# Kernel tuning notes

Measured on AMD Instinct MI355X. Metric: run time of the kernel, lower is better.

The kernel has to match this reference:

```python
import jax, jax.numpy as jnp
import numpy as np
from jax import lax

B, T, N = 256, 2048, 64  # batch, max_seq_len, num_tags


def setup_inputs() -> dict:
    key = jax.random.key(0)
    k1, k2, k3 = jax.random.split(key, 3)
    x = jax.random.normal(k1, (B, T, N), dtype=jnp.float32)
    seq_len = jax.random.randint(k2, (B,), 1, T + 1).astype(jnp.int32)
    trans = (jax.random.normal(k3, (N, N), dtype=jnp.float32) * 0.1)
    return {"x": x, "seq_len": seq_len, "trans": trans}


def reference(x, seq_len, trans):
    # Viterbi decode (tfa.text.crf_decode): returns (tags [B,T] int32, scores [B] float)
    Bv, Tv, Nv = x.shape
    alpha0 = x[:, 0]                                   # [B,N]
    xs = jnp.swapaxes(x[:, 1:], 0, 1)                  # [T-1,B,N]
    valid = jnp.arange(1, Tv)[:, None] < seq_len[None, :]  # [T-1,B]
    ident = jnp.arange(Nv, dtype=jnp.int32)

    def fwd(alpha, inp):
        x_t, v = inp
        # scores[b, prev, cur] = alpha[b, prev] + trans[prev, cur]
        sc = alpha[:, :, None] + trans[None]           # [B,N,N]
        bp = jnp.argmax(sc, axis=1).astype(jnp.int32)  # [B,N] best prev tag per cur
        new_alpha = jnp.max(sc, axis=1) + x_t          # [B,N]
        # steps beyond seq_len: carry state, identity backpointer
        alpha_n = jnp.where(v[:, None], new_alpha, alpha)
        bp = jnp.where(v[:, None], bp, ident[None, :])
        return alpha_n, bp

    alpha_f, bps = lax.scan(fwd, alpha0, (xs, valid))  # bps: [T-1,B,N]
    scores = jnp.max(alpha_f, axis=-1)                 # [B]
    last = jnp.argmax(alpha_f, axis=-1).astype(jnp.int32)  # [B] tag at last step

    def bwd(tag, bp):
        prev = jnp.take_along_axis(bp, tag[:, None], axis=1)[:, 0]
        return prev, tag  # emit tag at step t+1, carry tag at step t

    first, rest = lax.scan(bwd, last, bps, reverse=True)   # rest: [T-1,B]
    tags = jnp.concatenate([first[:, None], jnp.swapaxes(rest, 0, 1)], axis=1)  # [B,T]
    return tags, scores
```

## Files before the change

kernel.cpp:

```cpp
#include <hip/hip_runtime.h>

#define BB 256
#define TT 2048
#define NN 64
#define CHK 512

template <int K>
__device__ __forceinline__ int dpp_ror_i(int v) {
  return __builtin_amdgcn_update_dpp(0, v, 0x120 | K, 0xF, 0xF, true);
}
template <int K>
__device__ __forceinline__ float dpp_ror_f(float v) {
  return __int_as_float(dpp_ror_i<K>(__float_as_int(v)));
}

__device__ __forceinline__ float rowpair_max(float m) {
  int a = __float_as_int(m), b = a;
  asm volatile("v_permlane16_swap_b32 %0, %1" : "+v"(a), "+v"(b));
  float fa = __int_as_float(a), fb = __int_as_float(b);
  return fmaxf(fa, fb);
}
__device__ __forceinline__ float half_max(float m) {
  int a = __float_as_int(m), b = a;
  asm volatile("v_permlane32_swap_b32 %0, %1" : "+v"(a), "+v"(b));
  float fa = __int_as_float(a), fb = __int_as_float(b);
  return fmaxf(fa, fb);
}
__device__ __forceinline__ int rowpair_min(int v) {
  int a = v, b = v;
  asm volatile("v_permlane16_swap_b32 %0, %1" : "+v"(a), "+v"(b));
  return a < b ? a : b;
}
__device__ __forceinline__ int half_min(int v) {
  int a = v, b = v;
  asm volatile("v_permlane32_swap_b32 %0, %1" : "+v"(a), "+v"(b));
  return a < b ? a : b;
}

__global__ __launch_bounds__(256, 1)
void crf_viterbi_kernel(const float* __restrict__ x,
                        const int* __restrict__ seq_len,
                        const float* __restrict__ trans,
                        float* __restrict__ out) {
  const int b = blockIdx.x;
  const int tid = threadIdx.x;
  const int lane = tid & 63;
  const int w = tid >> 6;
  const int c = lane & 15;
  const int jc = (w << 4) + c;

  __shared__ __align__(16) float alpha_s[2][NN];
  __shared__ unsigned char bp_s[(TT - 1) * NN];
  __shared__ int map_s[4][NN];

  const float* xb = x + (size_t)b * TT * NN;
  const int slen = seq_len[b];

  int idxv[16];
  idxv[0] = lane;
  idxv[1] = dpp_ror_i<1>(lane);   idxv[2] = dpp_ror_i<2>(lane);
  idxv[3] = dpp_ror_i<3>(lane);   idxv[4] = dpp_ror_i<4>(lane);
  idxv[5] = dpp_ror_i<5>(lane);   idxv[6] = dpp_ror_i<6>(lane);
  idxv[7] = dpp_ror_i<7>(lane);   idxv[8] = dpp_ror_i<8>(lane);
  idxv[9] = dpp_ror_i<9>(lane);   idxv[10] = dpp_ror_i<10>(lane);
  idxv[11] = dpp_ror_i<11>(lane); idxv[12] = dpp_ror_i<12>(lane);
  idxv[13] = dpp_ror_i<13>(lane); idxv[14] = dpp_ror_i<14>(lane);
  idxv[15] = dpp_ror_i<15>(lane);

  float tcv[16];
#pragma unroll
  for (int k = 0; k < 16; ++k) tcv[k] = trans[idxv[k] * NN + jc];

  if (w == 0) alpha_s[0][lane] = xb[lane];
  __syncthreads();

  float xn1 = xb[NN + jc];
  float xn2 = xb[2 * NN + jc];

  for (int t = 1; t < slen; ++t) {
    float xv = xn1;
    xn1 = xn2;
    {
      int tn = (t + 2 < TT) ? (t + 2) : (TT - 1);
      xn2 = xb[(size_t)tn * NN + jc];
    }
    const int pr = (t + 1) & 1;
    const int pw = t & 1;

    float av = alpha_s[pr][lane];

    float c0 = av + tcv[0];
    float c1 = dpp_ror_f<1>(av) + tcv[1];
    float c2 = dpp_ror_f<2>(av) + tcv[2];
    float c3 = dpp_ror_f<3>(av) + tcv[3];
    float c4 = dpp_ror_f<4>(av) + tcv[4];
    float c5 = dpp_ror_f<5>(av) + tcv[5];
    float c6 = dpp_ror_f<6>(av) + tcv[6];
    float c7 = dpp_ror_f<7>(av) + tcv[7];
    float c8 = dpp_ror_f<8>(av) + tcv[8];
    float c9 = dpp_ror_f<9>(av) + tcv[9];
    float c10 = dpp_ror_f<10>(av) + tcv[10];
    float c11 = dpp_ror_f<11>(av) + tcv[11];
    float c12 = dpp_ror_f<12>(av) + tcv[12];
    float c13 = dpp_ror_f<13>(av) + tcv[13];
    float c14 = dpp_ror_f<14>(av) + tcv[14];
    float c15 = dpp_ror_f<15>(av) + tcv[15];

    float m = fmaxf(fmaxf(fmaxf(fmaxf(c0, c1), fmaxf(c2, c3)),
                          fmaxf(fmaxf(c4, c5), fmaxf(c6, c7))),
                    fmaxf(fmaxf(fmaxf(c8, c9), fmaxf(c10, c11)),
                          fmaxf(fmaxf(c12, c13), fmaxf(c14, c15))));
    m = rowpair_max(m);
    m = half_max(m);

    int s0 = (c0 == m) ? idxv[0] : NN;
    int s1 = (c1 == m) ? idxv[1] : NN;
    int s2 = (c2 == m) ? idxv[2] : NN;
    int s3 = (c3 == m) ? idxv[3] : NN;
    int s4 = (c4 == m) ? idxv[4] : NN;
    int s5 = (c5 == m) ? idxv[5] : NN;
    int s6 = (c6 == m) ? idxv[6] : NN;
    int s7 = (c7 == m) ? idxv[7] : NN;
    int s8 = (c8 == m) ? idxv[8] : NN;
    int s9 = (c9 == m) ? idxv[9] : NN;
    int s10 = (c10 == m) ? idxv[10] : NN;
    int s11 = (c11 == m) ? idxv[11] : NN;
    int s12 = (c12 == m) ? idxv[12] : NN;
    int s13 = (c13 == m) ? idxv[13] : NN;
    int s14 = (c14 == m) ? idxv[14] : NN;
    int s15 = (c15 == m) ? idxv[15] : NN;
    int idx = min(min(min(min(s0, s1), min(s2, s3)),
                      min(min(s4, s5), min(s6, s7))),
                  min(min(min(s8, s9), min(s10, s11)),
                      min(min(s12, s13), min(s14, s15))));
    idx = rowpair_min(idx);
    idx = half_min(idx);

    if (lane < 16) {
      alpha_s[pw][jc] = m + xv;
      bp_s[(t - 1) * NN + jc] = (unsigned char)idx;
    }
    asm volatile("s_waitcnt lgkmcnt(0)\n\ts_barrier" ::: "memory");
  }

  const int pf = (slen - 1) & 1;
  float best = alpha_s[pf][lane];
  int last = lane;
#pragma unroll
  for (int mask = 1; mask < 64; mask <<= 1) {
    float ov = __shfl_xor(best, mask, 64);
    int oi = __shfl_xor(last, mask, 64);
    bool take = (ov > best) || (ov == best && oi < last);
    best = take ? ov : best;
    last = take ? oi : last;
  }
  const float lastf = (float)last;
  const int bTT = b * TT;

  for (int t = slen - 1 + tid; t < TT; t += 256) out[bTT + t] = lastf;
  if (tid == 0) out[BB * TT + b] = best;

  const int lo = CHK * w;
  const int hi = ((CHK * (w + 1) - 1) < (slen - 2)) ? (CHK * (w + 1) - 1)
                                                    : (slen - 2);
  if (w > 0) {
    int s = lane;
    for (int r = hi; r >= lo; --r) s = bp_s[r * NN + s];
    map_s[w][lane] = s;
  }
  __syncthreads();

  const int e3 = last;
  const int e2 = map_s[3][e3];
  const int e1 = map_s[2][e2];
  const int e0 = map_s[1][e1];
  const int entry = (w == 3) ? e3 : (w == 2) ? e2 : (w == 1) ? e1 : e0;

  if (lane == 0) {
    int s = entry;
    for (int r = hi; r >= lo; --r) {
      s = bp_s[r * NN + s];
      out[bTT + r] = (float)s;
    }
  }
}

extern "C" void kernel_launch(void* const* d_in, const int* in_sizes, int n_in,
                              void* d_out, int out_size, void* d_ws, size_t ws_size,
                              hipStream_t stream) {
  const float* x = (const float*)d_in[0];
  const int* seq_len = (const int*)d_in[1];
  const float* trans = (const float*)d_in[2];
  float* out = (float*)d_out;

  crf_viterbi_kernel<<<BB, 256, 0, stream>>>(x, seq_len, trans, out);
}
```

Baseline: 805.1 us.

## Use single-wave forward pass storing alphas, recompute backpointers during backtrack

Adds a 64-thread-per-batch kernel that runs the forward max-plus recurrence in one wavefront, with no block barriers and no per-step argmax. It stores every alpha row to a global workspace. The backtrack then recomputes the argmax only along the chosen path, using a transposed trans copy in shared memory, wave reductions and a ballot. The old 4-wave kernel is kept as a fallback when the workspace is too small. This removes the argmax and barrier work from the serial loop, at the cost of a serial backtrack with a global load and a wave reduction per step, plus a large workspace write.

```diff
diff --git a/kernel.cpp b/kernel.cpp
--- a/kernel.cpp
+++ b/kernel.cpp
@@ -3,45 +3,162 @@
 #define BB 256
 #define TT 2048
 #define NN 64
-#define CHK 512
 
 template <int K>
-__device__ __forceinline__ int dpp_ror_i(int v) {
+__device__ __forceinline__ int rot_i(int v) {
   return __builtin_amdgcn_update_dpp(0, v, 0x120 | K, 0xF, 0xF, true);
 }
 template <int K>
-__device__ __forceinline__ float dpp_ror_f(float v) {
-  return __int_as_float(dpp_ror_i<K>(__float_as_int(v)));
-}
-
-__device__ __forceinline__ float rowpair_max(float m) {
+__device__ __forceinline__ float rot_f(float v) {
+  return __int_as_float(rot_i<K>(__float_as_int(v)));
+}
+__device__ __forceinline__ float pair16_max(float m) {
   int a = __float_as_int(m), b = a;
   asm volatile("v_permlane16_swap_b32 %0, %1" : "+v"(a), "+v"(b));
-  float fa = __int_as_float(a), fb = __int_as_float(b);
-  return fmaxf(fa, fb);
-}
-__device__ __forceinline__ float half_max(float m) {
+  return fmaxf(__int_as_float(a), __int_as_float(b));
+}
+__device__ __forceinline__ float pair32_max(float m) {
   int a = __float_as_int(m), b = a;
   asm volatile("v_permlane32_swap_b32 %0, %1" : "+v"(a), "+v"(b));
-  float fa = __int_as_float(a), fb = __int_as_float(b);
-  return fmaxf(fa, fb);
-}
-__device__ __forceinline__ int rowpair_min(int v) {
+  return fmaxf(__int_as_float(a), __int_as_float(b));
+}
+__device__ __forceinline__ int pair16_min(int v) {
   int a = v, b = v;
   asm volatile("v_permlane16_swap_b32 %0, %1" : "+v"(a), "+v"(b));
   return a < b ? a : b;
 }
-__device__ __forceinline__ int half_min(int v) {
+__device__ __forceinline__ int pair32_min(int v) {
   int a = v, b = v;
   asm volatile("v_permlane32_swap_b32 %0, %1" : "+v"(a), "+v"(b));
   return a < b ? a : b;
 }
+__device__ __forceinline__ float wave_max64(float v) {
+  float m = v;
+  m = fmaxf(m, rot_f<8>(m));
+  m = fmaxf(m, rot_f<4>(m));
+  m = fmaxf(m, rot_f<2>(m));
+  m = fmaxf(m, rot_f<1>(m));
+  m = pair16_max(m);
+  m = pair32_max(m);
+  return m;
+}
+
+__global__ __launch_bounds__(64, 1)
+void crf_viterbi_fast(const float* __restrict__ x,
+                      const int* __restrict__ seq_len,
+                      const float* __restrict__ trans,
+                      float* __restrict__ out,
+                      float* __restrict__ hist) {
+  const int b = blockIdx.x;
+  const int lane = threadIdx.x;
+
+  __shared__ float alp[2][NN];
+  __shared__ float transT[NN * 65];
+
+  const float* xb = x + (size_t)b * TT * NN;
+  float* hb = hist + (size_t)b * TT * NN;
+  const int slen = seq_len[b];
+  const int bTT = b * TT;
+
+  for (int r = 0; r < NN; ++r) transT[lane * 65 + r] = trans[r * NN + lane];
+
+  float tc0[16], tc1[16], tc2[16], tc3[16];
+  {
+    int s = lane;
+    tc0[0] = trans[s * NN + lane];
+    tc1[0] = trans[(s ^ 16) * NN + lane];
+    tc2[0] = trans[(s ^ 32) * NN + lane];
+    tc3[0] = trans[(s ^ 48) * NN + lane];
+  }
+#define TCL(K) { int s = rot_i<K>(lane);            \
+    tc0[K] = trans[s * NN + lane];                   \
+    tc1[K] = trans[(s ^ 16) * NN + lane];            \
+    tc2[K] = trans[(s ^ 32) * NN + lane];            \
+    tc3[K] = trans[(s ^ 48) * NN + lane]; }
+  TCL(1) TCL(2) TCL(3) TCL(4) TCL(5) TCL(6) TCL(7) TCL(8)
+  TCL(9) TCL(10) TCL(11) TCL(12) TCL(13) TCL(14) TCL(15)
+#undef TCL
+
+  float av = xb[lane];
+  hb[lane] = av;
+  alp[0][lane] = av;
+  float xn1 = xb[NN + lane];
+  float xn2 = xb[2 * NN + lane];
+  float xn3 = xb[3 * NN + lane];
+
+  for (int t = 1; t < slen; ++t) {
+    asm volatile("" ::: "memory");
+
+    const int pr = (t + 1) & 1;
+    float w1 = alp[pr][lane ^ 16];
+    float w2 = alp[pr][lane ^ 32];
+    float w3 = alp[pr][lane ^ 48];
+
+    float xv = xn1; xn1 = xn2; xn2 = xn3;
+    {
+      int tn = (t + 3 < TT) ? (t + 3) : (TT - 1);
+      xn3 = xb[(size_t)tn * NN + lane];
+    }
+
+#define Q(K) fmaxf(fmaxf(rot_f<K>(av) + tc0[K], rot_f<K>(w1) + tc1[K]), \
+                   fmaxf(rot_f<K>(w2) + tc2[K], rot_f<K>(w3) + tc3[K]))
+    float m0 = fmaxf(fmaxf(av + tc0[0], w1 + tc1[0]),
+                     fmaxf(w2 + tc2[0], w3 + tc3[0]));
+    float m1 = Q(1), m2 = Q(2), m3 = Q(3);
+    m0 = fmaxf(m0, Q(4));  m1 = fmaxf(m1, Q(5));
+    m2 = fmaxf(m2, Q(6));  m3 = fmaxf(m3, Q(7));
+    m0 = fmaxf(m0, Q(8));  m1 = fmaxf(m1, Q(9));
+    m2 = fmaxf(m2, Q(10)); m3 = fmaxf(m3, Q(11));
+    m0 = fmaxf(m0, Q(12)); m1 = fmaxf(m1, Q(13));
+    m2 = fmaxf(m2, Q(14)); m3 = fmaxf(m3, Q(15));
+#undef Q
+    float m = fmaxf(fmaxf(m0, m1), fmaxf(m2, m3));
+    av = m + xv;
+
+    alp[t & 1][lane] = av;
+    hb[(size_t)t * NN + lane] = av;
+  }
+
+  const float best = wave_max64(av);
+  const int last = ((int)__builtin_ctzll(__ballot(av == best))) & 63;
+
+  for (int t = slen - 1 + lane; t < TT; t += NN) out[bTT + t] = (float)last;
+  if (lane == 0) out[BB * TT + b] = best;
+
+  int start = slen - 2;
+  if (start >= 0) {
+    asm volatile("s_waitcnt vmcnt(0)" ::: "memory");
+    int tag = last;
+#define LDR(ROW) hb[(size_t)(((ROW) > 0) ? (ROW) : 0) * NN + lane]
+    float r0 = LDR(start), r1 = LDR(start - 1), r2 = LDR(start - 2),
+          r3 = LDR(start - 3);
+    int t = start;
+#define TSTEP(RREG, TIDX) {                                            \
+      float val = (RREG) + transT[tag * 65 + lane];                    \
+      float mm = wave_max64(val);                                      \
+      tag = ((int)__builtin_ctzll(__ballot(val == mm))) & 63;          \
+      if (lane == 0) out[bTT + (TIDX)] = (float)tag;                   \
+    }
+    while (t >= 3) {
+      TSTEP(r0, t);     r0 = LDR(t - 4);
+      TSTEP(r1, t - 1); r1 = LDR(t - 5);
+      TSTEP(r2, t - 2); r2 = LDR(t - 6);
+      TSTEP(r3, t - 3); r3 = LDR(t - 7);
+      t -= 4;
+    }
+    if (t >= 0) TSTEP(r0, t);
+    if (t >= 1) TSTEP(r1, t - 1);
+    if (t >= 2) TSTEP(r2, t - 2);
+#undef TSTEP
+#undef LDR
+  }
+}
 
 __global__ __launch_bounds__(256, 1)
-void crf_viterbi_kernel(const float* __restrict__ x,
-                        const int* __restrict__ seq_len,
-                        const float* __restrict__ trans,
-                        float* __restrict__ out) {
+void crf_viterbi_fb(const float* __restrict__ x,
+                    const int* __restrict__ seq_len,
+                    const float* __restrict__ trans,
+                    float* __restrict__ out) {
   const int b = blockIdx.x;
   const int tid = threadIdx.x;
   const int lane = tid & 63;
@@ -58,14 +175,14 @@
 
   int idxv[16];
   idxv[0] = lane;
-  idxv[1] = dpp_ror_i<1>(lane);   idxv[2] = dpp_ror_i<2>(lane);
-  idxv[3] = dpp_ror_i<3>(lane);   idxv[4] = dpp_ror_i<4>(lane);
-  idxv[5] = dpp_ror_i<5>(lane);   idxv[6] = dpp_ror_i<6>(lane);
-  idxv[7] = dpp_ror_i<7>(lane);   idxv[8] = dpp_ror_i<8>(lane);
-  idxv[9] = dpp_ror_i<9>(lane);   idxv[10] = dpp_ror_i<10>(lane);
-  idxv[11] = dpp_ror_i<11>(lane); idxv[12] = dpp_ror_i<12>(lane);
-  idxv[13] = dpp_ror_i<13>(lane); idxv[14] = dpp_ror_i<14>(lane);
-  idxv[15] = dpp_ror_i<15>(lane);
+  idxv[1] = rot_i<1>(lane);   idxv[2] = rot_i<2>(lane);
+  idxv[3] = rot_i<3>(lane);   idxv[4] = rot_i<4>(lane);
+  idxv[5] = rot_i<5>(lane);   idxv[6] = rot_i<6>(lane);
+  idxv[7] = rot_i<7>(lane);   idxv[8] = rot_i<8>(lane);
+  idxv[9] = rot_i<9>(lane);   idxv[10] = rot_i<10>(lane);
+  idxv[11] = rot_i<11>(lane); idxv[12] = rot_i<12>(lane);
+  idxv[13] = rot_i<13>(lane); idxv[14] = rot_i<14>(lane);
+  idxv[15] = rot_i<15>(lane);
 
   float tcv[16];
 #pragma unroll
@@ -87,31 +204,31 @@
     const int pr = (t + 1) & 1;
     const int pw = t & 1;
 
-    float av = alpha_s[pr][lane];
-
-    float c0 = av + tcv[0];
-    float c1 = dpp_ror_f<1>(av) + tcv[1];
-    float c2 = dpp_ror_f<2>(av) + tcv[2];
-    float c3 = dpp_ror_f<3>(av) + tcv[3];
-    float c4 = dpp_ror_f<4>(av) + tcv[4];
-    float c5 = dpp_ror_f<5>(av) + tcv[5];
-    float c6 = dpp_ror_f<6>(av) + tcv[6];
-    float c7 = dpp_ror_f<7>(av) + tcv[7];
-    float c8 = dpp_ror_f<8>(av) + tcv[8];
-    float c9 = dpp_ror_f<9>(av) + tcv[9];
-    float c10 = dpp_ror_f<10>(av) + tcv[10];
-    float c11 = dpp_ror_f<11>(av) + tcv[11];
-    float c12 = dpp_ror_f<12>(av) + tcv[12];
-    float c13 = dpp_ror_f<13>(av) + tcv[13];
-    float c14 = dpp_ror_f<14>(av) + tcv[14];
-    float c15 = dpp_ror_f<15>(av) + tcv[15];
+    float avf = alpha_s[pr][lane];
+
+    float c0 = avf + tcv[0];
+    float c1 = rot_f<1>(avf) + tcv[1];
+    float c2 = rot_f<2>(avf) + tcv[2];
+    float c3 = rot_f<3>(avf) + tcv[3];
+    float c4 = rot_f<4>(avf) + tcv[4];
+    float c5 = rot_f<5>(avf) + tcv[5];
+    float c6 = rot_f<6>(avf) + tcv[6];
+    float c7 = rot_f<7>(avf) + tcv[7];
+    float c8 = rot_f<8>(avf) + tcv[8];
+    float c9 = rot_f<9>(avf) + tcv[9];
+    float c10 = rot_f<10>(avf) + tcv[10];
+    float c11 = rot_f<11>(avf) + tcv[11];
+    float c12 = rot_f<12>(avf) + tcv[12];
+    float c13 = rot_f<13>(avf) + tcv[13];
+    float c14 = rot_f<14>(avf) + tcv[14];
+    float c15 = rot_f<15>(avf) + tcv[15];
 
     float m = fmaxf(fmaxf(fmaxf(fmaxf(c0, c1), fmaxf(c2, c3)),
                           fmaxf(fmaxf(c4, c5), fmaxf(c6, c7))),
                     fmaxf(fmaxf(fmaxf(c8, c9), fmaxf(c10, c11)),
                           fmaxf(fmaxf(c12, c13), fmaxf(c14, c15))));
-    m = rowpair_max(m);
-    m = half_max(m);
+    m = pair16_max(m);
+    m = pair32_max(m);
 
     int s0 = (c0 == m) ? idxv[0] : NN;
     int s1 = (c1 == m) ? idxv[1] : NN;
@@ -133,8 +250,8 @@
                       min(min(s4, s5), min(s6, s7))),
                   min(min(min(s8, s9), min(s10, s11)),
                       min(min(s12, s13), min(s14, s15))));
-    idx = rowpair_min(idx);
-    idx = half_min(idx);
+    idx = pair16_min(idx);
+    idx = pair32_min(idx);
 
     if (lane < 16) {
       alpha_s[pw][jc] = m + xv;
@@ -160,8 +277,8 @@
   for (int t = slen - 1 + tid; t < TT; t += 256) out[bTT + t] = lastf;
   if (tid == 0) out[BB * TT + b] = best;
 
-  const int lo = CHK * w;
-  const int hi = ((CHK * (w + 1) - 1) < (slen - 2)) ? (CHK * (w + 1) - 1)
+  const int lo = 512 * w;
+  const int hi = ((512 * (w + 1) - 1) < (slen - 2)) ? (512 * (w + 1) - 1)
                                                     : (slen - 2);
   if (w > 0) {
     int s = lane;
@@ -193,5 +310,11 @@
   const float* trans = (const float*)d_in[2];
   float* out = (float*)d_out;
 
-  crf_viterbi_kernel<<<BB, 256, 0, stream>>>(x, seq_len, trans, out);
-}
+  const size_t need = (size_t)BB * TT * NN * sizeof(float);
+  if (ws_size >= need) {
+    crf_viterbi_fast<<<BB, 64, 0, stream>>>(x, seq_len, trans, out,
+                                            (float*)d_ws);
+  } else {
+    crf_viterbi_fb<<<BB, 256, 0, stream>>>(x, seq_len, trans, out);
+  }
+}
```

Measured after the change: 914.5 us. 13.6% more time.
